# Kernel optimization log

Hardware: AMD Instinct MI355X
Metric: run time of the kernel (lower is better)

## Reference

```python
import jax, jax.numpy as jnp
import numpy as np

N_NODES = 40000
N_EDGES = 640000
N_FEAT = 128
HIDDEN = 128
N_GRAPHS = 64


def _sage_conv(x, src, dst, Wl, b, Wr):
    # PyG SAGEConv (aggr='mean', root_weight=True, normalize=False):
    # out_i = W_l @ mean_{j in N(i)} x_j + b + W_r @ x_i
    msg = x[src]                                             # [E, F]
    s = jax.ops.segment_sum(msg, dst, num_segments=N_NODES)  # [N, F]
    deg = jax.ops.segment_sum(jnp.ones((src.shape[0],), x.dtype), dst,
                              num_segments=N_NODES)
    agg = s / jnp.maximum(deg, 1.0)[:, None]
    return agg @ Wl + b + x @ Wr


def setup_inputs() -> dict:
    key = jax.random.key(0)
    ks = jax.random.split(key, 12)
    sc = 1.0 / np.sqrt(N_FEAT)
    x = jax.random.normal(ks[0], (N_NODES, N_FEAT), dtype=jnp.float32)
    edge_index = jax.random.randint(ks[1], (2, N_EDGES), 0, N_NODES, dtype=jnp.int32)
    batch = jnp.sort(jax.random.randint(ks[2], (N_NODES,), 0, N_GRAPHS, dtype=jnp.int32))
    mk = lambda k, shp: (jax.random.normal(k, shp, dtype=jnp.float32) * sc)
    return {
        'x': x, 'edge_index': edge_index, 'batch': batch,
        'W1l': mk(ks[3], (N_FEAT, HIDDEN)), 'b1': jnp.zeros((HIDDEN,), jnp.float32),
        'W1r': mk(ks[4], (N_FEAT, HIDDEN)),
        'W2l': mk(ks[5], (HIDDEN, HIDDEN)), 'b2': jnp.zeros((HIDDEN,), jnp.float32),
        'W2r': mk(ks[6], (HIDDEN, HIDDEN)),
        'W3l': mk(ks[7], (HIDDEN, HIDDEN)), 'b3': jnp.zeros((HIDDEN,), jnp.float32),
        'W3r': mk(ks[8], (HIDDEN, HIDDEN)),
        'Wlin': mk(ks[9], (3 * HIDDEN, HIDDEN)), 'blin': jnp.zeros((HIDDEN,), jnp.float32),
    }


def reference(x, edge_index, batch, W1l, b1, W1r, W2l, b2, W2r, W3l, b3, W3r, Wlin, blin):
    src, dst = edge_index[0], edge_index[1]
    h1 = jax.nn.relu(_sage_conv(x, src, dst, W1l, b1, W1r))
    h2 = jax.nn.relu(_sage_conv(h1, src, dst, W2l, b2, W2r))
    h3 = jax.nn.relu(_sage_conv(h2, src, dst, W3l, b3, W3r))
    h = jnp.concatenate([h1, h2, h3], axis=1)                # [N, 3*H]
    pooled = jax.ops.segment_sum(h, batch, num_segments=N_GRAPHS)  # global_add_pool
    out = jax.nn.relu(pooled @ Wlin + blin)                  # [G, H]
    return out
```

## Files before the change

kernel.cpp:

```cpp
#include <hip/hip_runtime.h>
#include <hip/hip_bf16.h>

#define N_NODES 40000
#define N_EDGES 640000
#define NFEAT 128
#define NGRAPHS 64
#define ECAP 1536

typedef __attribute__((ext_vector_type(8))) short short8;
typedef __attribute__((ext_vector_type(4))) float float4v;

static __device__ __forceinline__ float bf2f(unsigned short u) {
    unsigned int x = ((unsigned int)u) << 16;
    return __builtin_bit_cast(float, x);
}
static __device__ __forceinline__ unsigned short f2bf(float f) {
    unsigned int x = __builtin_bit_cast(unsigned int, f);
    unsigned int r = x + 0x7fffu + ((x >> 16) & 1u);
    return (unsigned short)(r >> 16);
}

__global__ void k_prep(const int* __restrict__ dst, int* __restrict__ deg,
                       const int* __restrict__ batch, int* __restrict__ goff,
                       const float* __restrict__ x, unsigned short* __restrict__ h0,
                       const float* __restrict__ Wl0, const float* __restrict__ Wr0,
                       const float* __restrict__ Wl1, const float* __restrict__ Wr1,
                       const float* __restrict__ Wl2, const float* __restrict__ Wr2,
                       unsigned short* __restrict__ Wt) {
    int b = blockIdx.x;
    if (b < 2500) {
        int e = b * 256 + threadIdx.x;
        if (e < N_EDGES) atomicAdd(&deg[dst[e]], 1);
    } else if (b < 2657) {
        int i = (b - 2500) * 256 + threadIdx.x;
        if (i >= N_NODES) return;
        int b1 = batch[i];
        int b0 = (i == 0) ? -1 : batch[i - 1];
        for (int g = b0 + 1; g <= b1; ++g) goff[g] = i;
        if (i == N_NODES - 1)
            for (int g = b1 + 1; g <= NGRAPHS; ++g) goff[g] = N_NODES;
    } else if (b < 12657) {
        int i = (b - 2657) * 256 + threadIdx.x;
        const int n = N_NODES * NFEAT / 2;
        if (i < n) {
            float a = x[2 * i], c = x[2 * i + 1];
            unsigned int u = (unsigned int)f2bf(a) | ((unsigned int)f2bf(c) << 16);
            ((unsigned int*)h0)[i] = u;
        }
    } else {
        int id = (b - 12657) * 256 + threadIdx.x;
        if (id >= 3 * 128 * 256) return;
        int l   = id >> 15;
        int rem = id & 32767;
        int nn  = rem >> 8;
        int k   = rem & 255;
        const float* Wl = (l == 0) ? Wl0 : (l == 1) ? Wl1 : Wl2;
        const float* Wr = (l == 0) ? Wr0 : (l == 1) ? Wr1 : Wr2;
        float v = (k < 128) ? Wl[k * 128 + nn] : Wr[(k - 128) * 128 + nn];
        Wt[id] = f2bf(v);
    }
}

__global__ __launch_bounds__(1024) void k_scan(const int* __restrict__ deg,
                                               int* __restrict__ offsets,
                                               int* __restrict__ cursor) {
    __shared__ int ws[16];
    __shared__ int s_boff;
    int tid = threadIdx.x;
    int b = blockIdx.x;
    int lane = tid & 63, wave = tid >> 6;

    int lim = b << 10;
    int s = 0;
    for (int i = tid; i < lim; i += 1024) s += deg[i];
    for (int d = 1; d < 64; d <<= 1) s += __shfl_xor(s, d, 64);
    if (lane == 0) ws[wave] = s;
    __syncthreads();
    if (tid == 0) {
        int t = 0;
        for (int w = 0; w < 16; ++w) t += ws[w];
        s_boff = t;
    }
    __syncthreads();
    int boff = s_boff;

    int i = (b << 10) + tid;
    int v = (i < N_NODES) ? deg[i] : 0;
    int incl = v;
    for (int d = 1; d < 64; d <<= 1) {
        int t = __shfl_up(incl, d, 64);
        if (lane >= d) incl += t;
    }
    __syncthreads();
    if (lane == 63) ws[wave] = incl;
    __syncthreads();
    if (wave == 0 && lane < 16) {
        int w = ws[lane];
        for (int d = 1; d < 16; d <<= 1) {
            int t = __shfl_up(w, d, 64);
            if (lane >= d) w += t;
        }
        ws[lane] = w;
    }
    __syncthreads();
    int waveOff = (wave == 0) ? 0 : ws[wave - 1];
    if (i < N_NODES) {
        int o = boff + waveOff + incl - v;
        offsets[i] = o;
        cursor[i]  = o;
    }
    if (b == 39 && tid == 0) offsets[N_NODES] = N_EDGES;
}

__global__ void k_fill(const int* __restrict__ src, const int* __restrict__ dst,
                       int* __restrict__ cursor, int* __restrict__ esrc) {
    int e = blockIdx.x * 256 + threadIdx.x;
    if (e < N_EDGES) {
        int d = dst[e];
        int p = atomicAdd(&cursor[d], 1);
        esrc[p] = src[e];
    }
}

__global__ __launch_bounds__(256) void k_sage(
        const unsigned short* __restrict__ hin,
        const int* __restrict__ offsets,
        const int* __restrict__ esrc,
        const unsigned short* __restrict__ Wt,
        const float* __restrict__ bias,
        unsigned short* __restrict__ hout) {
    __shared__ __align__(16) unsigned short As[64][264];
    __shared__ int eidx[ECAP];
    int tid = threadIdx.x;
    int row0 = blockIdx.x * 64;

    int estart = offsets[row0];
    int ecnt   = offsets[row0 + 64] - estart;
    int staged = ecnt < ECAP ? ecnt : ECAP;

    for (int p = 0; p < 4; ++p) {
        int ci = tid + p * 256;
        int r = ci >> 4, c8 = ci & 15;
        uint4 v = *(const uint4*)(hin + (size_t)(row0 + r) * 128 + c8 * 8);
        *(uint4*)(&As[r][128 + c8 * 8]) = v;
    }
    for (int t = tid; t < staged; t += 256) eidx[t] = esrc[estart + t];
    __syncthreads();

    {
        int grp = tid >> 4;
        int sub = tid & 15;
        for (int nn = 0; nn < 4; ++nn) {
            int r = nn * 16 + grp;
            int node = row0 + r;
            int beg = offsets[node], end = offsets[node + 1];
            float a[8];
            for (int i = 0; i < 8; ++i) a[i] = 0.f;
            auto acc8 = [&](uint4 u) {
                a[0] += bf2f((unsigned short)(u.x & 0xffffu));
                a[1] += bf2f((unsigned short)(u.x >> 16));
                a[2] += bf2f((unsigned short)(u.y & 0xffffu));
                a[3] += bf2f((unsigned short)(u.y >> 16));
                a[4] += bf2f((unsigned short)(u.z & 0xffffu));
                a[5] += bf2f((unsigned short)(u.z >> 16));
                a[6] += bf2f((unsigned short)(u.w & 0xffffu));
                a[7] += bf2f((unsigned short)(u.w >> 16));
            };
            if (end - estart <= staged) {
                int lj = beg - estart, lend = end - estart;
                for (; lj + 8 <= lend; lj += 8) {
                    int s0 = eidx[lj],     s1 = eidx[lj + 1];
                    int s2 = eidx[lj + 2], s3 = eidx[lj + 3];
                    int s4 = eidx[lj + 4], s5 = eidx[lj + 5];
                    int s6 = eidx[lj + 6], s7 = eidx[lj + 7];
                    uint4 u0 = *(const uint4*)(hin + (size_t)s0 * 128 + sub * 8);
                    uint4 u1 = *(const uint4*)(hin + (size_t)s1 * 128 + sub * 8);
                    uint4 u2 = *(const uint4*)(hin + (size_t)s2 * 128 + sub * 8);
                    uint4 u3 = *(const uint4*)(hin + (size_t)s3 * 128 + sub * 8);
                    uint4 u4 = *(const uint4*)(hin + (size_t)s4 * 128 + sub * 8);
                    uint4 u5 = *(const uint4*)(hin + (size_t)s5 * 128 + sub * 8);
                    uint4 u6 = *(const uint4*)(hin + (size_t)s6 * 128 + sub * 8);
                    uint4 u7 = *(const uint4*)(hin + (size_t)s7 * 128 + sub * 8);
                    acc8(u0); acc8(u1); acc8(u2); acc8(u3);
                    acc8(u4); acc8(u5); acc8(u6); acc8(u7);
                }
                for (; lj < lend; ++lj) {
                    int s = eidx[lj];
                    uint4 u = *(const uint4*)(hin + (size_t)s * 128 + sub * 8);
                    acc8(u);
                }
            } else {
                for (int j = beg; j < end; ++j) {
                    int s = esrc[j];
                    uint4 u = *(const uint4*)(hin + (size_t)s * 128 + sub * 8);
                    acc8(u);
                }
            }
            int deg = end - beg;
            float inv = 1.f / (float)(deg > 1 ? deg : 1);
            uint4 v;
            v.x = (unsigned int)f2bf(a[0] * inv) | ((unsigned int)f2bf(a[1] * inv) << 16);
            v.y = (unsigned int)f2bf(a[2] * inv) | ((unsigned int)f2bf(a[3] * inv) << 16);
            v.z = (unsigned int)f2bf(a[4] * inv) | ((unsigned int)f2bf(a[5] * inv) << 16);
            v.w = (unsigned int)f2bf(a[6] * inv) | ((unsigned int)f2bf(a[7] * inv) << 16);
            *(uint4*)(&As[r][sub * 8]) = v;
        }
    }
    __syncthreads();

    int wave = tid >> 6, lane = tid & 63;
    int quad = lane >> 4, l16 = lane & 15;
    float4v acc[4][2];
    for (int rt = 0; rt < 4; ++rt)
        for (int ct = 0; ct < 2; ++ct) acc[rt][ct] = {0.f, 0.f, 0.f, 0.f};

    int ncol0 = wave * 32;
    for (int kc = 0; kc < 8; ++kc) {
        int k0 = kc * 32 + quad * 8;
        short8 a[4], b[2];
        for (int rt = 0; rt < 4; ++rt)
            a[rt] = *(const short8*)(&As[rt * 16 + l16][k0]);
        for (int ct = 0; ct < 2; ++ct)
            b[ct] = *(const short8*)(Wt + (size_t)(ncol0 + ct * 16 + l16) * 256 + k0);
        for (int rt = 0; rt < 4; ++rt)
            for (int ct = 0; ct < 2; ++ct)
                acc[rt][ct] = __builtin_amdgcn_mfma_f32_16x16x32_bf16(
                    a[rt], b[ct], acc[rt][ct], 0, 0, 0);
    }

    for (int ct = 0; ct < 2; ++ct) {
        int col = ncol0 + ct * 16 + l16;
        float bv = bias[col];
        for (int rt = 0; rt < 4; ++rt) {
            int r0 = rt * 16 + quad * 4;
            for (int i = 0; i < 4; ++i) {
                float v = acc[rt][ct][i] + bv;
                v = v > 0.f ? v : 0.f;
                hout[(size_t)(row0 + r0 + i) * 128 + col] = f2bf(v);
            }
        }
    }
}

__global__ __launch_bounds__(256) void k_poolfinal(
        const unsigned short* __restrict__ h1,
        const unsigned short* __restrict__ h2,
        const unsigned short* __restrict__ h3,
        const int* __restrict__ goff,
        const float* __restrict__ Wlin,
        const float* __restrict__ blin,
        float* __restrict__ out) {
    __shared__ float red[4][16][8];
    __shared__ float pool_s[384];
    int g = blockIdx.x;
    int beg = goff[g], end = goff[g + 1];
    int tid = threadIdx.x;
    int rp = tid >> 4;
    int ch = tid & 15;
    int wave = tid >> 6, lane = tid & 63;

    for (int aidx = 0; aidx < 3; ++aidx) {
        const unsigned short* h = (aidx == 0) ? h1 : (aidx == 1) ? h2 : h3;
        float a[8];
        for (int i = 0; i < 8; ++i) a[i] = 0.f;
        for (int r = beg + rp; r < end; r += 16) {
            uint4 u = *(const uint4*)(h + (size_t)r * 128 + ch * 8);
            a[0] += bf2f((unsigned short)(u.x & 0xffffu));
            a[1] += bf2f((unsigned short)(u.x >> 16));
            a[2] += bf2f((unsigned short)(u.y & 0xffffu));
            a[3] += bf2f((unsigned short)(u.y >> 16));
            a[4] += bf2f((unsigned short)(u.z & 0xffffu));
            a[5] += bf2f((unsigned short)(u.z >> 16));
            a[6] += bf2f((unsigned short)(u.w & 0xffffu));
            a[7] += bf2f((unsigned short)(u.w >> 16));
        }
        for (int i = 0; i < 8; ++i) {
            a[i] += __shfl_xor(a[i], 16, 64);
            a[i] += __shfl_xor(a[i], 32, 64);
        }
        if (lane < 16)
            for (int i = 0; i < 8; ++i) red[wave][lane][i] = a[i];
        __syncthreads();
        if (tid < 128) {
            int ch2 = tid >> 3, e = tid & 7;
            pool_s[aidx * 128 + ch2 * 8 + e] =
                red[0][ch2][e] + red[1][ch2][e] + red[2][ch2][e] + red[3][ch2][e];
        }
        __syncthreads();
    }

    if (tid < 128) {
        float acc = blin[tid];
        for (int k = 0; k < 384; ++k)
            acc = fmaf(pool_s[k], Wlin[k * 128 + tid], acc);
        out[g * 128 + tid] = acc > 0.f ? acc : 0.f;
    }
}

extern "C" void kernel_launch(void* const* d_in, const int* in_sizes, int n_in,
                              void* d_out, int out_size, void* d_ws, size_t ws_size,
                              hipStream_t stream) {
    const float* x    = (const float*)d_in[0];
    const int*   ei   = (const int*)d_in[1];
    const int*   src  = ei;
    const int*   dst  = ei + N_EDGES;
    const int*   batch = (const int*)d_in[2];
    const float* W1l = (const float*)d_in[3];
    const float* b1  = (const float*)d_in[4];
    const float* W1r = (const float*)d_in[5];
    const float* W2l = (const float*)d_in[6];
    const float* b2  = (const float*)d_in[7];
    const float* W2r = (const float*)d_in[8];
    const float* W3l = (const float*)d_in[9];
    const float* b3  = (const float*)d_in[10];
    const float* W3r = (const float*)d_in[11];
    const float* Wlin = (const float*)d_in[12];
    const float* blin = (const float*)d_in[13];
    float* out = (float*)d_out;

    char* ws = (char*)d_ws;
    size_t off = 0;
    auto alloc = [&](size_t bytes) -> char* {
        char* p = ws + off;
        off = (off + bytes + 255) & ~(size_t)255;
        return p;
    };
    int* offsets = (int*)alloc((N_NODES + 1) * sizeof(int));
    int* cursor  = (int*)alloc(N_NODES * sizeof(int));
    int* deg     = (int*)alloc(N_NODES * sizeof(int));
    int* goff    = (int*)alloc((NGRAPHS + 1) * sizeof(int));
    int* esrc    = (int*)alloc(N_EDGES * sizeof(int));
    unsigned short* h0   = (unsigned short*)alloc((size_t)N_NODES * 128 * 2);
    unsigned short* h1   = (unsigned short*)alloc((size_t)N_NODES * 128 * 2);
    unsigned short* h2   = (unsigned short*)alloc((size_t)N_NODES * 128 * 2);
    unsigned short* h3   = (unsigned short*)alloc((size_t)N_NODES * 128 * 2);
    unsigned short* Wt   = (unsigned short*)alloc(3 * 256 * 128 * 2);

    hipMemsetAsync(deg, 0, N_NODES * sizeof(int), stream);

    k_prep<<<13041, 256, 0, stream>>>(dst, deg, batch, goff, x, h0,
                                      W1l, W1r, W2l, W2r, W3l, W3r, Wt);
    k_scan<<<40, 1024, 0, stream>>>(deg, offsets, cursor);
    k_fill<<<(N_EDGES + 255) / 256, 256, 0, stream>>>(src, dst, cursor, esrc);

    k_sage<<<625, 256, 0, stream>>>(h0, offsets, esrc, Wt,             b1, h1);
    k_sage<<<625, 256, 0, stream>>>(h1, offsets, esrc, Wt + 32768,     b2, h2);
    k_sage<<<625, 256, 0, stream>>>(h2, offsets, esrc, Wt + 2 * 32768, b3, h3);

    k_poolfinal<<<NGRAPHS, 256, 0, stream>>>(h1, h2, h3, goff, Wlin, blin, out);
}
```

Baseline: 297.9 us.

## Halve SAGE row tile and split pooling into parallel pool and final kernels

The SAGE kernel now handles 32 rows per block instead of 64, with smaller shared tiles and an occupancy hint, doubling the grid to 1250 blocks. This gives the 256 CUs more blocks and waves to hide gather latency, but each block reloads weight fragments for half as many rows. Pooling is split into 192 blocks (one per graph and layer) writing to a workspace buffer, followed by a small final linear kernel. This raises parallelism in a stage that ran only 64 blocks, at the cost of one extra launch.

```diff
diff --git a/kernel.cpp b/kernel.cpp
--- a/kernel.cpp
+++ b/kernel.cpp
@@ -5,7 +5,7 @@
 #define N_EDGES 640000
 #define NFEAT 128
 #define NGRAPHS 64
-#define ECAP 1536
+#define ECAP 1024
 
 typedef __attribute__((ext_vector_type(8))) short short8;
 typedef __attribute__((ext_vector_type(4))) float float4v;
@@ -122,23 +122,23 @@
     }
 }
 
-__global__ __launch_bounds__(256) void k_sage(
+__global__ __launch_bounds__(256, 7) void k_sage(
         const unsigned short* __restrict__ hin,
         const int* __restrict__ offsets,
         const int* __restrict__ esrc,
         const unsigned short* __restrict__ Wt,
         const float* __restrict__ bias,
         unsigned short* __restrict__ hout) {
-    __shared__ __align__(16) unsigned short As[64][264];
+    __shared__ __align__(16) unsigned short As[32][264];
     __shared__ int eidx[ECAP];
     int tid = threadIdx.x;
-    int row0 = blockIdx.x * 64;
+    int row0 = blockIdx.x * 32;
 
     int estart = offsets[row0];
-    int ecnt   = offsets[row0 + 64] - estart;
+    int ecnt   = offsets[row0 + 32] - estart;
     int staged = ecnt < ECAP ? ecnt : ECAP;
 
-    for (int p = 0; p < 4; ++p) {
+    for (int p = 0; p < 2; ++p) {
         int ci = tid + p * 256;
         int r = ci >> 4, c8 = ci & 15;
         uint4 v = *(const uint4*)(hin + (size_t)(row0 + r) * 128 + c8 * 8);
@@ -150,7 +150,7 @@
     {
         int grp = tid >> 4;
         int sub = tid & 15;
-        for (int nn = 0; nn < 4; ++nn) {
+        for (int nn = 0; nn < 2; ++nn) {
             int r = nn * 16 + grp;
             int node = row0 + r;
             int beg = offsets[node], end = offsets[node + 1];
@@ -210,19 +210,19 @@
 
     int wave = tid >> 6, lane = tid & 63;
     int quad = lane >> 4, l16 = lane & 15;
-    float4v acc[4][2];
-    for (int rt = 0; rt < 4; ++rt)
+    float4v acc[2][2];
+    for (int rt = 0; rt < 2; ++rt)
         for (int ct = 0; ct < 2; ++ct) acc[rt][ct] = {0.f, 0.f, 0.f, 0.f};
 
     int ncol0 = wave * 32;
     for (int kc = 0; kc < 8; ++kc) {
         int k0 = kc * 32 + quad * 8;
-        short8 a[4], b[2];
-        for (int rt = 0; rt < 4; ++rt)
+        short8 a[2], b[2];
+        for (int rt = 0; rt < 2; ++rt)
             a[rt] = *(const short8*)(&As[rt * 16 + l16][k0]);
         for (int ct = 0; ct < 2; ++ct)
             b[ct] = *(const short8*)(Wt + (size_t)(ncol0 + ct * 16 + l16) * 256 + k0);
-        for (int rt = 0; rt < 4; ++rt)
+        for (int rt = 0; rt < 2; ++rt)
             for (int ct = 0; ct < 2; ++ct)
                 acc[rt][ct] = __builtin_amdgcn_mfma_f32_16x16x32_bf16(
                     a[rt], b[ct], acc[rt][ct], 0, 0, 0);
@@ -231,7 +231,7 @@
     for (int ct = 0; ct < 2; ++ct) {
         int col = ncol0 + ct * 16 + l16;
         float bv = bias[col];
-        for (int rt = 0; rt < 4; ++rt) {
+        for (int rt = 0; rt < 2; ++rt) {
             int r0 = rt * 16 + quad * 4;
             for (int i = 0; i < 4; ++i) {
                 float v = acc[rt][ct][i] + bv;
@@ -242,59 +242,56 @@
     }
 }
 
-__global__ __launch_bounds__(256) void k_poolfinal(
-        const unsigned short* __restrict__ h1,
-        const unsigned short* __restrict__ h2,
-        const unsigned short* __restrict__ h3,
-        const int* __restrict__ goff,
-        const float* __restrict__ Wlin,
-        const float* __restrict__ blin,
-        float* __restrict__ out) {
+__global__ __launch_bounds__(256) void k_pool(const unsigned short* __restrict__ h1,
+                                              const unsigned short* __restrict__ h2,
+                                              const unsigned short* __restrict__ h3,
+                                              const int* __restrict__ goff,
+                                              float* __restrict__ pooled) {
     __shared__ float red[4][16][8];
-    __shared__ float pool_s[384];
-    int g = blockIdx.x;
+    int b = blockIdx.x;
+    int g = b / 3, aidx = b % 3;
+    const unsigned short* h = (aidx == 0) ? h1 : (aidx == 1) ? h2 : h3;
     int beg = goff[g], end = goff[g + 1];
     int tid = threadIdx.x;
     int rp = tid >> 4;
     int ch = tid & 15;
+    float a[8];
+    for (int i = 0; i < 8; ++i) a[i] = 0.f;
+    for (int r = beg + rp; r < end; r += 16) {
+        uint4 u = *(const uint4*)(h + (size_t)r * 128 + ch * 8);
+        a[0] += bf2f((unsigned short)(u.x & 0xffffu));
+        a[1] += bf2f((unsigned short)(u.x >> 16));
+        a[2] += bf2f((unsigned short)(u.y & 0xffffu));
+        a[3] += bf2f((unsigned short)(u.y >> 16));
+        a[4] += bf2f((unsigned short)(u.z & 0xffffu));
+        a[5] += bf2f((unsigned short)(u.z >> 16));
+        a[6] += bf2f((unsigned short)(u.w & 0xffffu));
+        a[7] += bf2f((unsigned short)(u.w >> 16));
+    }
+    for (int i = 0; i < 8; ++i) {
+        a[i] += __shfl_xor(a[i], 16, 64);
+        a[i] += __shfl_xor(a[i], 32, 64);
+    }
     int wave = tid >> 6, lane = tid & 63;
-
-    for (int aidx = 0; aidx < 3; ++aidx) {
-        const unsigned short* h = (aidx == 0) ? h1 : (aidx == 1) ? h2 : h3;
-        float a[8];
-        for (int i = 0; i < 8; ++i) a[i] = 0.f;
-        for (int r = beg + rp; r < end; r += 16) {
-            uint4 u = *(const uint4*)(h + (size_t)r * 128 + ch * 8);
-            a[0] += bf2f((unsigned short)(u.x & 0xffffu));
-            a[1] += bf2f((unsigned short)(u.x >> 16));
-            a[2] += bf2f((unsigned short)(u.y & 0xffffu));
-            a[3] += bf2f((unsigned short)(u.y >> 16));
-            a[4] += bf2f((unsigned short)(u.z & 0xffffu));
-            a[5] += bf2f((unsigned short)(u.z >> 16));
-            a[6] += bf2f((unsigned short)(u.w & 0xffffu));
-            a[7] += bf2f((unsigned short)(u.w >> 16));
-        }
-        for (int i = 0; i < 8; ++i) {
-            a[i] += __shfl_xor(a[i], 16, 64);
-            a[i] += __shfl_xor(a[i], 32, 64);
-        }
-        if (lane < 16)
-            for (int i = 0; i < 8; ++i) red[wave][lane][i] = a[i];
-        __syncthreads();
-        if (tid < 128) {
-            int ch2 = tid >> 3, e = tid & 7;
-            pool_s[aidx * 128 + ch2 * 8 + e] =
-                red[0][ch2][e] + red[1][ch2][e] + red[2][ch2][e] + red[3][ch2][e];
-        }
-        __syncthreads();
-    }
-
+    if (lane < 16)
+        for (int i = 0; i < 8; ++i) red[wave][lane][i] = a[i];
+    __syncthreads();
     if (tid < 128) {
-        float acc = blin[tid];
-        for (int k = 0; k < 384; ++k)
-            acc = fmaf(pool_s[k], Wlin[k * 128 + tid], acc);
-        out[g * 128 + tid] = acc > 0.f ? acc : 0.f;
-    }
+        int ch2 = tid >> 3, e = tid & 7;
+        float s = red[0][ch2][e] + red[1][ch2][e] + red[2][ch2][e] + red[3][ch2][e];
+        pooled[g * 384 + aidx * 128 + ch2 * 8 + e] = s;
+    }
+}
+
+__global__ void k_final(const float* __restrict__ pooled,
+                        const float* __restrict__ Wlin,
+                        const float* __restrict__ blin,
+                        float* __restrict__ out) {
+    int g = blockIdx.x, col = threadIdx.x;
+    float acc = blin[col];
+    for (int k = 0; k < 384; ++k)
+        acc = fmaf(pooled[g * 384 + k], Wlin[k * 128 + col], acc);
+    out[g * 128 + col] = acc > 0.f ? acc : 0.f;
 }
 
 extern "C" void kernel_launch(void* const* d_in, const int* in_sizes, int n_in,
@@ -335,6 +332,7 @@
     unsigned short* h2   = (unsigned short*)alloc((size_t)N_NODES * 128 * 2);
     unsigned short* h3   = (unsigned short*)alloc((size_t)N_NODES * 128 * 2);
     unsigned short* Wt   = (unsigned short*)alloc(3 * 256 * 128 * 2);
+    float* pooled = (float*)alloc(NGRAPHS * 384 * sizeof(float));
 
     hipMemsetAsync(deg, 0, N_NODES * sizeof(int), stream);
 
@@ -343,9 +341,10 @@
     k_scan<<<40, 1024, 0, stream>>>(deg, offsets, cursor);
     k_fill<<<(N_EDGES + 255) / 256, 256, 0, stream>>>(src, dst, cursor, esrc);
 
-    k_sage<<<625, 256, 0, stream>>>(h0, offsets, esrc, Wt,             b1, h1);
-    k_sage<<<625, 256, 0, stream>>>(h1, offsets, esrc, Wt + 32768,     b2, h2);
-    k_sage<<<625, 256, 0, stream>>>(h2, offsets, esrc, Wt + 2 * 32768, b3, h3);
-
-    k_poolfinal<<<NGRAPHS, 256, 0, stream>>>(h1, h2, h3, goff, Wlin, blin, out);
-}
+    k_sage<<<1250, 256, 0, stream>>>(h0, offsets, esrc, Wt,             b1, h1);
+    k_sage<<<1250, 256, 0, stream>>>(h1, offsets, esrc, Wt + 32768,     b2, h2);
+    k_sage<<<1250, 256, 0, stream>>>(h2, offsets, esrc, Wt + 2 * 32768, b3, h3);
+
+    k_pool<<<3 * NGRAPHS, 256, 0, stream>>>(h1, h2, h3, goff, pooled);
+    k_final<<<NGRAPHS, 128, 0, stream>>>(pooled, Wlin, blin, out);
+}
```

Result: faster. 274.5 us (-7.9%).
